# Optimization experiments

Measured on AMD Instinct MI355X. Metric: run time of the kernel, lower is better.

The kernel has to match this reference:

```python
import jax, jax.numpy as jnp
import numpy as np

B, S, D = 4, 2048, 1024
H, DK, DV = 16, 64, 64


def setup_inputs() -> dict:
    key = jax.random.key(0)
    ks = jax.random.split(key, 12)
    s = 0.02
    return {
        "inputEmbeddings_Q": jax.random.normal(ks[0], (B, S, D), jnp.float32),
        "inputEmbeddings_K": jax.random.normal(ks[1], (B, S, D), jnp.float32),
        "inputEmbeddings_V": jax.random.normal(ks[2], (B, S, D), jnp.float32),
        "attentionMask": jax.random.randint(ks[3], (B, S, S), 0, 2) > 0,
        "Wq": jax.random.normal(ks[4], (D, H * DK), jnp.float32) * s,
        "bq": jnp.zeros((H * DK,), jnp.float32),
        "Wk": jax.random.normal(ks[5], (D, H * DK), jnp.float32) * s,
        "bk": jnp.zeros((H * DK,), jnp.float32),
        "Wv": jax.random.normal(ks[6], (D, H * DV), jnp.float32) * s,
        "bv": jnp.zeros((H * DV,), jnp.float32),
        "Wo": jax.random.normal(ks[7], (H * DV, D), jnp.float32) * s,
        "bo": jnp.zeros((D,), jnp.float32),
        "ln_gamma": jnp.ones((D,), jnp.float32),
        "ln_beta": jnp.zeros((D,), jnp.float32),
    }


def _layer_norm(x, gamma, beta, eps=1e-5):
    mu = jnp.mean(x, axis=-1, keepdims=True)
    var = jnp.var(x, axis=-1, keepdims=True)
    return (x - mu) * jax.lax.rsqrt(var + eps) * gamma + beta


def reference(inputEmbeddings_Q, inputEmbeddings_K, inputEmbeddings_V, attentionMask,
              Wq, bq, Wk, bk, Wv, bv, Wo, bo, ln_gamma, ln_beta):
    residual = inputEmbeddings_Q
    b = inputEmbeddings_Q.shape[0]
    # projections -> [B, H, S, d]
    q = (inputEmbeddings_Q @ Wq + bq).reshape(b, -1, H, DK).transpose(0, 2, 1, 3)
    k = (inputEmbeddings_K @ Wk + bk).reshape(b, -1, H, DK).transpose(0, 2, 1, 3)
    v = (inputEmbeddings_V @ Wv + bv).reshape(b, -1, H, DV).transpose(0, 2, 1, 3)
    scores = jnp.einsum("bhqd,bhkd->bhqk", q, k) / np.sqrt(DK).astype(np.float32)
    scores = jnp.where(attentionMask[:, None, :, :], jnp.float32(-1e9), scores)
    attention = jax.nn.softmax(scores, axis=-1)  # [B,H,Sq,Sk]
    context = jnp.einsum("bhqk,bhkd->bhqd", attention, v)
    context = context.transpose(0, 2, 1, 3).reshape(b, -1, H * DV)
    output = context @ Wo + bo
    output = _layer_norm(output + residual, ln_gamma, ln_beta)
    return output, attention
```

## Files before the change

### kernel.cpp

```cpp
#include <hip/hip_runtime.h>

typedef unsigned short u16;
typedef unsigned int u32;
typedef __bf16 bf16x8 __attribute__((ext_vector_type(8)));
typedef __bf16 bf16x4 __attribute__((ext_vector_type(4)));
typedef u16 u16x8 __attribute__((ext_vector_type(8)));
typedef u32 u32x2 __attribute__((ext_vector_type(2)));
typedef u32 u32x4 __attribute__((ext_vector_type(4)));
typedef float f32x4 __attribute__((ext_vector_type(4)));

#define Ss 2048
#define Hh 16

#define WAITV(n) asm volatile("s_waitcnt vmcnt(" #n ")" ::: "memory")
#define BAR() __builtin_amdgcn_s_barrier()
#define SCHED0() __builtin_amdgcn_sched_barrier(0)

__device__ __forceinline__ void gll16(const void* g, void* l) {
  __builtin_amdgcn_global_load_lds((const __attribute__((address_space(1))) void*)g,
                                   (__attribute__((address_space(3))) void*)l, 16, 0, 0);
}

__device__ __forceinline__ bf16x8 lds8(const u16* base, int byteoff) {
  return __builtin_bit_cast(bf16x8, *(const u16x8*)((const char*)base + byteoff));
}
__device__ __forceinline__ bf16x4 lds4(const u16* base, int byteoff) {
  return __builtin_bit_cast(bf16x4, *(const unsigned long long*)((const char*)base + byteoff));
}
__device__ __forceinline__ bf16x8 g8(const u16* p) {
  return __builtin_bit_cast(bf16x8, *(const u16x8*)p);
}
__device__ __forceinline__ u16 bfbits(float f) {
  return __builtin_bit_cast(u16, (__bf16)f);
}

__global__ __launch_bounds__(256) void convert_x(const float* __restrict__ xq,
                                                 const float* __restrict__ xk,
                                                 const float* __restrict__ xv,
                                                 u16* __restrict__ dst) {
  int z = blockIdx.y;
  const float* src = (z == 0) ? xq : ((z == 1) ? xk : xv);
  u16* d = dst + (size_t)z * (8192ull * 1024);
  size_t i = ((size_t)blockIdx.x * 256 + threadIdx.x) * 8;
  float4 v0 = *(const float4*)(src + i);
  float4 v1 = *(const float4*)(src + i + 4);
  bf16x8 o;
  o[0] = (__bf16)v0.x; o[1] = (__bf16)v0.y; o[2] = (__bf16)v0.z; o[3] = (__bf16)v0.w;
  o[4] = (__bf16)v1.x; o[5] = (__bf16)v1.y; o[6] = (__bf16)v1.z; o[7] = (__bf16)v1.w;
  *(bf16x8*)(d + i) = o;
}

__global__ __launch_bounds__(256) void conv_w(const float* __restrict__ wq,
                                              const float* __restrict__ wk,
                                              const float* __restrict__ wv,
                                              const float* __restrict__ wo,
                                              u16* __restrict__ wt) {
  int z = blockIdx.z;
  const float* W = (z == 0) ? wq : (z == 1) ? wk : (z == 2) ? wv : wo;
  u16* O = wt + (size_t)z * (1024ull * 1024);
  __shared__ float tile[64][65];
  int tk = blockIdx.x * 64, tn = blockIdx.y * 64;
  int t = threadIdx.x;
#pragma unroll
  for (int p = 0; p < 4; ++p) {
    int idx = p * 256 + t;
    int r = idx >> 4, c4 = (idx & 15) << 2;
    float4 v = *(const float4*)(W + (size_t)(tk + r) * 1024 + tn + c4);
    tile[r][c4 + 0] = v.x; tile[r][c4 + 1] = v.y;
    tile[r][c4 + 2] = v.z; tile[r][c4 + 3] = v.w;
  }
  __syncthreads();
#pragma unroll
  for (int p = 0; p < 4; ++p) {
    int idx = p * 256 + t;
    int n = idx >> 4, k4 = (idx & 15) << 2;
    bf16x4 o;
    o[0] = (__bf16)tile[k4 + 0][n]; o[1] = (__bf16)tile[k4 + 1][n];
    o[2] = (__bf16)tile[k4 + 2][n]; o[3] = (__bf16)tile[k4 + 3][n];
    *(bf16x4*)(O + (size_t)(tn + n) * 1024 + tk + k4) = o;
  }
}

__global__ __launch_bounds__(256) void pack_mask(const int* __restrict__ m,
                                                 u32* __restrict__ bits) {
  size_t base = (size_t)blockIdx.x * 512;
  int t = threadIdx.x;
  int w = t >> 6, lane = t & 63;
  bool v0 = (m[base + t] != 0);
  bool v1 = (m[base + 256 + t] != 0);
  unsigned long long b0 = __ballot(v0);
  unsigned long long b1 = __ballot(v1);
  size_t wbase = (base >> 5) + (w << 1);
  if (lane == 0) {
    bits[wbase] = (u32)b0;
    bits[wbase + 8] = (u32)b1;
  } else if (lane == 32) {
    bits[wbase + 1] = (u32)(b0 >> 32);
    bits[wbase + 9] = (u32)(b1 >> 32);
  }
}

__global__ __launch_bounds__(256) void gemm_qkv(const u16* __restrict__ Xbf,
                                                const u16* __restrict__ Wt,
                                                const float* __restrict__ bq,
                                                const float* __restrict__ bk,
                                                const float* __restrict__ bv,
                                                u16* __restrict__ OutQK,
                                                u16* __restrict__ Vt) {
  int z = blockIdx.z;
  const u16* A = Xbf + (size_t)z * (8192ull * 1024);
  const u16* Bw = Wt + (size_t)z * (1024ull * 1024);
  const float* bias = (z == 0) ? bq : ((z == 1) ? bk : bv);
  u16* O = OutQK + (size_t)z * (8192ull * 1024);
  float scale = (z == 0) ? (0.125f * 1.4426950408889634f) : 1.0f;

  __shared__ __attribute__((aligned(16))) u16 SM[16384];

  int t = threadIdx.x, w = t >> 6, l = t & 63, lg = l >> 4, lr = l & 15;
  int n_ = blockIdx.x;
  int cx = n_ & 7, slot = n_ >> 3;
  int m0 = (((slot >> 3) << 3) | cx) * 128;
  int n0 = (slot & 7) * 128;
  int wm = (w >> 1) * 64, wn = (w & 1) * 64;

  f32x4 acc[4][4] = {};

#define STAGE_AB(kt_, buf_)                                                    \
  {                                                                            \
    _Pragma("unroll") for (int i = 0; i < 2; ++i) {                            \
      int c = t + i * 256;                                                     \
      int d = c << 4;                                                          \
      int row = d >> 6, off = d & 63;                                          \
      int soff = off ^ ((row & 3) << 4);                                       \
      gll16(A + (size_t)(m0 + row) * 1024 + (kt_) + (soff >> 1),               \
            (char*)SM + (buf_)*8192 + d);                                      \
      gll16(Bw + (size_t)(n0 + row) * 1024 + (kt_) + (soff >> 1),              \
            (char*)SM + 16384 + (buf_)*8192 + d);                              \
    }                                                                          \
  }

  STAGE_AB(0, 0);

  for (int tt = 0; tt < 32; ++tt) {
    int cur = tt & 1;
    if (tt < 31) {
      STAGE_AB((tt + 1) * 32, cur ^ 1);
      WAITV(4);
    } else {
      WAITV(0);
    }
    SCHED0();
    BAR();
    const u16* Ac = SM + cur * 4096;
    const u16* Bc = SM + 8192 + cur * 4096;
    bf16x8 af[4], bfr[4];
#pragma unroll
    for (int mf = 0; mf < 4; ++mf) {
      int row = wm + mf * 16 + lr;
      af[mf] = lds8(Ac, (row << 6) + ((lg ^ (row & 3)) << 4));
    }
#pragma unroll
    for (int nf = 0; nf < 4; ++nf) {
      int row = wn + nf * 16 + lr;
      bfr[nf] = lds8(Bc, (row << 6) + ((lg ^ (row & 3)) << 4));
    }
#pragma unroll
    for (int mf = 0; mf < 4; ++mf)
#pragma unroll
      for (int nf = 0; nf < 4; ++nf)
        acc[mf][nf] = __builtin_amdgcn_mfma_f32_16x16x32_bf16(af[mf], bfr[nf], acc[mf][nf], 0, 0, 0);
    BAR();
  }
#undef STAGE_AB

  if (z == 2) {
#pragma unroll
    for (int mf = 0; mf < 4; ++mf)
#pragma unroll
      for (int nf = 0; nf < 4; ++nf) {
        int mloc = wm + mf * 16 + lg * 4;
        int nloc = wn + nf * 16 + lr;
        bf16x4 ov;
        int n = n0 + nloc;
#pragma unroll
        for (int r = 0; r < 4; ++r) ov[r] = (__bf16)(acc[mf][nf][r] + bias[n]);
        *(bf16x4*)&SM[nloc * 128 + (mloc ^ ((nloc & 7) << 3))] = ov;
      }
    BAR();
    int b_ = m0 >> 11, s0_ = m0 & 2047;
#pragma unroll
    for (int i = 0; i < 8; ++i) {
      int idx = i * 256 + t;
      int nloc = idx >> 4, c = idx & 15;
      u16x8 val = *(const u16x8*)&SM[nloc * 128 + (((c ^ (nloc & 7)) << 3))];
      int n = n0 + nloc, hh = n >> 6, dd = n & 63;
      *(u16x8*)&Vt[(((size_t)(b_ * 16 + hh)) * 64 + dd) * 2048 + s0_ + c * 8] = val;
    }
  } else {
#pragma unroll
    for (int mf = 0; mf < 4; ++mf)
#pragma unroll
      for (int nf = 0; nf < 4; ++nf)
#pragma unroll
        for (int r = 0; r < 4; ++r) {
          int row = wm + mf * 16 + lg * 4 + r;
          int col = wn + nf * 16 + lr;
          float v = (acc[mf][nf][r] + bias[n0 + col]) * scale;
          SM[row * 128 + (col ^ ((row & 7) << 3))] = bfbits(v);
        }
    BAR();
    int b_ = m0 >> 11, s0_ = m0 & 2047;
#pragma unroll
    for (int i = 0; i < 8; ++i) {
      int idx = i * 256 + t;
      int row = idx >> 4, c = idx & 15;
      u16x8 val = *(const u16x8*)&SM[row * 128 + (((c ^ (row & 7)) << 3))];
      int n = n0 + c * 8, hh = n >> 6, dd = n & 63;
      *(u16x8*)&O[(((size_t)(b_ * 16 + hh)) * 2048 + s0_ + row) * 64 + dd] = val;
    }
  }
}

__global__ __launch_bounds__(256, 4) void attn_kernel(const u16* __restrict__ Qs,
                                                      const u16* __restrict__ Ks,
                                                      const u16* __restrict__ Vt,
                                                      const u32* __restrict__ Mbits,
                                                      float* __restrict__ attn,
                                                      u16* __restrict__ Ctx) {
  int bid = blockIdx.x;
  int xcd = bid & 7, j = bid >> 3;
  int bh = xcd * 8 + (j >> 5);
  int q0 = (j & 31) * 64;
  int b = bh >> 4, h = bh & 15;
  int t = threadIdx.x;
  int w = t >> 6, l = t & 63, lg = l >> 4, lr = l & 15;

  const u16* Qb = Qs + (size_t)bh * (Ss * 64);
  const u16* Kb = Ks + (size_t)bh * (Ss * 64);
  const u16* Vb = Vt + (size_t)bh * (64 * Ss);
  int qrow = w * 16 + lr;
  const u32* Mrow = Mbits + ((size_t)b * Ss + q0 + qrow) * 64;

  __shared__ __attribute__((aligned(16))) char SMb[40960];
  u16* Pl = (u16*)(SMb + 32768);

  int srow = t >> 3;
  int skoff = (((t & 7) << 4) ^ ((srow & 7) << 4));

#define STAGE_K2(kc_, buf_)                                                    \
  {                                                                            \
    _Pragma("unroll") for (int i = 0; i < 4; ++i)                              \
        gll16(Kb + (size_t)((kc_) + srow + 32 * i) * 64 + (skoff >> 1),        \
              SMb + (buf_)*16384 + i * 4096 + (t << 4));                       \
  }
#define STAGE_K(kc_, buf_)                                                     \
  {                                                                            \
    gll16(Kb + (size_t)((kc_) + srow) * 64 + (skoff >> 1),                     \
          SMb + (buf_)*8192 + (t << 4));                                       \
    gll16(Kb + (size_t)((kc_) + srow + 32) * 64 + (skoff >> 1),                \
          SMb + (buf_)*8192 + (t << 4) + 4096);                                \
  }
#define STAGE_V(kc_, buf_)                                                     \
  {                                                                            \
    gll16(Vb + (size_t)srow * 2048 + (kc_) + (skoff >> 1),                     \
          SMb + 16384 + (buf_)*8192 + (t << 4));                               \
    gll16(Vb + (size_t)(srow + 32) * 2048 + (kc_) + (skoff >> 1),              \
          SMb + 16384 + (buf_)*8192 + (t << 4) + 4096);                        \
  }

  bf16x8 qf[2];
  {
    const u16* qr = Qb + (size_t)(q0 + qrow) * 64;
    qf[0] = g8(qr + lg * 8);
    qf[1] = g8(qr + 32 + lg * 8);
  }

  int swzq = (lr & 7) << 4;

  float rsum = 0.f;
  {
    STAGE_K2(0, 0);
    u32x4 mq = *(const u32x4*)(Mrow);
    u32x4 mqn;
    for (int tt = 0; tt < 16; ++tt) {
      int cur = tt & 1;
      if (tt < 15) {
        STAGE_K2((tt + 1) * 128, cur ^ 1);
        mqn = *(const u32x4*)(Mrow + ((tt + 1) << 2));
        WAITV(5);
      } else {
        WAITV(0);
      }
      SCHED0();
      BAR();
      const u16* Kc = (const u16*)(SMb + cur * 16384);
#pragma unroll
      for (int nf = 0; nf < 8; ++nf) {
        int krow = nf * 16 + lr;
        int base = krow << 7, swz = (krow & 7) << 4;
        f32x4 sc = {};
        __builtin_amdgcn_s_setprio(1);
        sc = __builtin_amdgcn_mfma_f32_16x16x32_bf16(
            lds8(Kc, base + ((lg << 4) ^ swz)), qf[0], sc, 0, 0, 0);
        sc = __builtin_amdgcn_mfma_f32_16x16x32_bf16(
            lds8(Kc, base + ((64 + (lg << 4)) ^ swz)), qf[1], sc, 0, 0, 0);
        __builtin_amdgcn_s_setprio(0);
        u32 mb = mq[nf >> 1] >> (((nf & 1) << 4) + (lg << 2));
#pragma unroll
        for (int r = 0; r < 4; ++r)
          rsum += ((mb >> r) & 1) ? 0.f : __builtin_amdgcn_exp2f(sc[r]);
      }
      mq = mqn;
      BAR();
    }
  }
  float inv;
  {
    float s = rsum;
    s += __shfl_xor(s, 16);
    s += __shfl_xor(s, 32);
    inv = 1.0f / s;
  }

  float* abase = attn + ((size_t)bh * Ss + q0 + w * 16) * Ss;
  int rsub = l >> 4;
  int kch = (l & 15);
  f32x4 ctx[4] = {};
  {
    STAGE_K(0, 0);
    STAGE_V(0, 0);
    u32x2 mq = *(const u32x2*)(Mrow);
    u32x2 mqn;
    for (int tt = 0; tt < 32; ++tt) {
      int cur = tt & 1;
      if (tt == 0) {
        STAGE_K(64, 1);
        STAGE_V(64, 1);
        mqn = *(const u32x2*)(Mrow + 2);
        WAITV(5);
      } else if (tt < 31) {
        STAGE_K((tt + 1) * 64, cur ^ 1);
        STAGE_V((tt + 1) * 64, cur ^ 1);
        mqn = *(const u32x2*)(Mrow + ((tt + 1) << 1));
        WAITV(9);
      } else {
        WAITV(4);
      }
      SCHED0();
      BAR();
      const u16* Kc = (const u16*)(SMb + cur * 8192);
      const u16* Vc = (const u16*)(SMb + 16384 + cur * 8192);
      int kc = tt * 64;
#pragma unroll
      for (int nf = 0; nf < 4; ++nf) {
        int krow = nf * 16 + lr;
        int base = krow << 7, swz = (krow & 7) << 4;
        f32x4 sc = {};
        __builtin_amdgcn_s_setprio(1);
        sc = __builtin_amdgcn_mfma_f32_16x16x32_bf16(
            lds8(Kc, base + ((lg << 4) ^ swz)), qf[0], sc, 0, 0, 0);
        sc = __builtin_amdgcn_mfma_f32_16x16x32_bf16(
            lds8(Kc, base + ((64 + (lg << 4)) ^ swz)), qf[1], sc, 0, 0, 0);
        __builtin_amdgcn_s_setprio(0);
        u32 mb = mq[nf >> 1] >> (((nf & 1) << 4) + (lg << 2));
        f32x4 p4;
#pragma unroll
        for (int r = 0; r < 4; ++r)
          p4[r] = (((mb >> r) & 1) ? 0.f : __builtin_amdgcn_exp2f(sc[r])) * inv;
        bf16x4 pb;
#pragma unroll
        for (int r = 0; r < 4; ++r) pb[r] = (__bf16)p4[r];
        *(bf16x4*)((char*)Pl + (qrow << 7) + (((nf << 5) + (lg << 3)) ^ swzq)) = pb;
      }
#pragma unroll
      for (int rb = 0; rb < 4; ++rb) {
        int rrow = rb * 4 + rsub;
        int R = w * 16 + rrow;
        bf16x4 pv4 = lds4(Pl, (R << 7) + ((kch << 3) ^ ((R & 7) << 4)));
        f32x4 o4;
#pragma unroll
        for (int r = 0; r < 4; ++r) o4[r] = (float)pv4[r];
        __builtin_nontemporal_store(
            o4, (f32x4*)(abase + (size_t)rrow * Ss + kc + kch * 4));
      }
      __builtin_amdgcn_s_setprio(1);
#pragma unroll
      for (int ks = 0; ks < 2; ++ks) {
        bf16x8 pf = lds8(Pl, (qrow << 7) + (((ks << 6) + (lg << 4)) ^ swzq));
#pragma unroll
        for (int nfo = 0; nfo < 4; ++nfo) {
          int vr = nfo * 16 + lr;
          bf16x8 vf = lds8(Vc,
                           (vr << 7) + (((ks << 6) + (lg << 4)) ^ ((vr & 7) << 4)));
          ctx[nfo] = __builtin_amdgcn_mfma_f32_16x16x32_bf16(pf, vf, ctx[nfo], 0, 0, 0);
        }
      }
      __builtin_amdgcn_s_setprio(0);
      mq = mqn;
      BAR();
    }
  }
#undef STAGE_K2
#undef STAGE_K
#undef STAGE_V

  {
    u16* Cl = (u16*)SMb + w * 1024;
#pragma unroll
    for (int nfo = 0; nfo < 4; ++nfo)
#pragma unroll
      for (int r = 0; r < 4; ++r)
        Cl[(lg * 4 + r) * 64 + nfo * 16 + lr] = bfbits(ctx[nfo][r]);
#pragma unroll
    for (int i = 0; i < 2; ++i) {
      int row = (l >> 3) + (i << 3);
      u16x8 cv = *(const u16x8*)(Cl + row * 64 + (l & 7) * 8);
      *(u16x8*)&Ctx[((size_t)b * Ss + q0 + w * 16 + row) * 1024 + h * 64 +
                    (l & 7) * 8] = cv;
    }
  }
}

__global__ __launch_bounds__(256) void gemm_out(const u16* __restrict__ Ctx,
                                                const u16* __restrict__ Wot,
                                                const float* __restrict__ bo,
                                                const float* __restrict__ resid,
                                                float* __restrict__ preLN) {
  __shared__ __attribute__((aligned(16))) u16 Al[2][128 * 32];
  __shared__ __attribute__((aligned(16))) u16 Bl[2][128 * 32];

  int t = threadIdx.x, w = t >> 6, l = t & 63, lg = l >> 4, lr = l & 15;
  int n_ = blockIdx.x;
  int cx = n_ & 7, slot = n_ >> 3;
  int m0 = (((slot >> 3) << 3) | cx) * 128;
  int n0 = (slot & 7) * 128;
  int wm = (w >> 1) * 64, wn = (w & 1) * 64;

  f32x4 acc[4][4] = {};

#define STAGE_AB(kt_, buf_)                                                    \
  {                                                                            \
    _Pragma("unroll") for (int i = 0; i < 2; ++i) {                            \
      int c = t + i * 256;                                                     \
      int d = c << 4;                                                          \
      int row = d >> 6, off = d & 63;                                          \
      int soff = off ^ ((row & 3) << 4);                                       \
      gll16(Ctx + (size_t)(m0 + row) * 1024 + (kt_) + (soff >> 1),             \
            (char*)Al[buf_] + d);                                              \
      gll16(Wot + (size_t)(n0 + row) * 1024 + (kt_) + (soff >> 1),             \
            (char*)Bl[buf_] + d);                                              \
    }                                                                          \
  }

  STAGE_AB(0, 0);

  for (int tt = 0; tt < 32; ++tt) {
    int cur = tt & 1;
    if (tt < 31) {
      STAGE_AB((tt + 1) * 32, cur ^ 1);
      WAITV(4);
    } else {
      WAITV(0);
    }
    SCHED0();
    BAR();
    bf16x8 af[4], bfr[4];
#pragma unroll
    for (int mf = 0; mf < 4; ++mf) {
      int row = wm + mf * 16 + lr;
      af[mf] = lds8(Al[cur], (row << 6) + ((lg ^ (row & 3)) << 4));
    }
#pragma unroll
    for (int nf = 0; nf < 4; ++nf) {
      int row = wn + nf * 16 + lr;
      bfr[nf] = lds8(Bl[cur], (row << 6) + ((lg ^ (row & 3)) << 4));
    }
#pragma unroll
    for (int mf = 0; mf < 4; ++mf)
#pragma unroll
      for (int nf = 0; nf < 4; ++nf)
        acc[mf][nf] = __builtin_amdgcn_mfma_f32_16x16x32_bf16(af[mf], bfr[nf], acc[mf][nf], 0, 0, 0);
    BAR();
  }
#undef STAGE_AB

#pragma unroll
  for (int mf = 0; mf < 4; ++mf)
#pragma unroll
    for (int nf = 0; nf < 4; ++nf)
#pragma unroll
      for (int r = 0; r < 4; ++r) {
        int m = m0 + wm + mf * 16 + lg * 4 + r;
        int n = n0 + wn + nf * 16 + lr;
        float v = acc[mf][nf][r] + bo[n] + resid[(size_t)m * 1024 + n];
        preLN[(size_t)m * 1024 + n] = v;
      }
}

__global__ __launch_bounds__(256) void layernorm(const float* __restrict__ x,
                                                 const float* __restrict__ gamma,
                                                 const float* __restrict__ beta,
                                                 float* __restrict__ out) {
  int t = threadIdx.x;
  int w = t >> 6, l = t & 63;
  int row = blockIdx.x * 4 + w;
  const float* xr = x + (size_t)row * 1024;
  float4 v[4];
  float s = 0.f, s2 = 0.f;
#pragma unroll
  for (int c = 0; c < 4; ++c) {
    v[c] = *(const float4*)(xr + c * 256 + l * 4);
    s += v[c].x + v[c].y + v[c].z + v[c].w;
    s2 += v[c].x * v[c].x + v[c].y * v[c].y + v[c].z * v[c].z + v[c].w * v[c].w;
  }
#pragma unroll
  for (int m = 1; m < 64; m <<= 1) {
    s += __shfl_xor(s, m);
    s2 += __shfl_xor(s2, m);
  }
  float mu = s * (1.0f / 1024.0f);
  float var = s2 * (1.0f / 1024.0f) - mu * mu;
  float rs = rsqrtf(var + 1e-5f);
  float* orow = out + (size_t)row * 1024;
#pragma unroll
  for (int c = 0; c < 4; ++c) {
    float4 g = *(const float4*)(gamma + c * 256 + l * 4);
    float4 bb = *(const float4*)(beta + c * 256 + l * 4);
    float4 o;
    o.x = (v[c].x - mu) * rs * g.x + bb.x;
    o.y = (v[c].y - mu) * rs * g.y + bb.y;
    o.z = (v[c].z - mu) * rs * g.z + bb.z;
    o.w = (v[c].w - mu) * rs * g.w + bb.w;
    *(float4*)(orow + c * 256 + l * 4) = o;
  }
}

extern "C" void kernel_launch(void* const* d_in, const int* in_sizes, int n_in,
                              void* d_out, int out_size, void* d_ws, size_t ws_size,
                              hipStream_t stream) {
  const float* Xq = (const float*)d_in[0];
  const float* Xk = (const float*)d_in[1];
  const float* Xv = (const float*)d_in[2];
  const int* Mask = (const int*)d_in[3];
  const float* Wq = (const float*)d_in[4];
  const float* bq = (const float*)d_in[5];
  const float* Wk = (const float*)d_in[6];
  const float* bk = (const float*)d_in[7];
  const float* Wv = (const float*)d_in[8];
  const float* bv = (const float*)d_in[9];
  const float* Wo = (const float*)d_in[10];
  const float* bo = (const float*)d_in[11];
  const float* gamma = (const float*)d_in[12];
  const float* beta = (const float*)d_in[13];

  char* ws = (char*)d_ws;
  u16* Xbf   = (u16*)(ws + 0);
  u16* Wt    = (u16*)(ws + 50331648);
  u16* Qs    = (u16*)(ws + 58720256);
  u16* Vt    = (u16*)(ws + 92274688);
  u32* Mbits = (u32*)(ws + 109051904);
  u16* Ctx   = (u16*)(ws + 111149056);
  float* preLN = (float*)(ws + 0);

  u16* Ks = Qs + 8192ull * 1024;

  float* outp = (float*)d_out;
  float* attn = outp + 8388608ull;

  (void)in_sizes; (void)n_in; (void)out_size; (void)ws_size;

  convert_x<<<dim3(4096, 3), 256, 0, stream>>>(Xq, Xk, Xv, Xbf);
  conv_w<<<dim3(16, 16, 4), 256, 0, stream>>>(Wq, Wk, Wv, Wo, Wt);
  pack_mask<<<32768, 256, 0, stream>>>(Mask, Mbits);
  gemm_qkv<<<dim3(512, 1, 3), 256, 0, stream>>>(Xbf, Wt, bq, bk, bv, Qs, Vt);
  attn_kernel<<<2048, 256, 0, stream>>>(Qs, Ks, Vt, Mbits, attn, Ctx);
  gemm_out<<<512, 256, 0, stream>>>(Ctx, Wt + 3ull * 1048576, bo, Xq, preLN);
  layernorm<<<2048, 256, 0, stream>>>(preLN, gamma, beta, outp);
}
```

Baseline: 390.5 us.

## Merge prep kernels into one launch and store pre-LayerNorm output as bf16

Combines the input conversion, weight transpose-conversion and mask packing into a single kernel dispatched by block index, with nontemporal loads for the K/V inputs and the mask. gemm_out now stages its tile through LDS, adds the residual with coalesced vector loads, and writes the pre-LayerNorm values as bf16 instead of fp32. LayerNorm reads the bf16 buffer. This removes two launches and halves the pre-LN traffic, but rounding to bf16 twice before the normalisation lowers accuracy.

```diff
diff --git a/kernel.cpp b/kernel.cpp
--- a/kernel.cpp
+++ b/kernel.cpp
@@ -34,69 +34,77 @@
   return __builtin_bit_cast(u16, (__bf16)f);
 }
 
-__global__ __launch_bounds__(256) void convert_x(const float* __restrict__ xq,
-                                                 const float* __restrict__ xk,
-                                                 const float* __restrict__ xv,
-                                                 u16* __restrict__ dst) {
-  int z = blockIdx.y;
-  const float* src = (z == 0) ? xq : ((z == 1) ? xk : xv);
-  u16* d = dst + (size_t)z * (8192ull * 1024);
-  size_t i = ((size_t)blockIdx.x * 256 + threadIdx.x) * 8;
-  float4 v0 = *(const float4*)(src + i);
-  float4 v1 = *(const float4*)(src + i + 4);
-  bf16x8 o;
-  o[0] = (__bf16)v0.x; o[1] = (__bf16)v0.y; o[2] = (__bf16)v0.z; o[3] = (__bf16)v0.w;
-  o[4] = (__bf16)v1.x; o[5] = (__bf16)v1.y; o[6] = (__bf16)v1.z; o[7] = (__bf16)v1.w;
-  *(bf16x8*)(d + i) = o;
-}
-
-__global__ __launch_bounds__(256) void conv_w(const float* __restrict__ wq,
-                                              const float* __restrict__ wk,
-                                              const float* __restrict__ wv,
-                                              const float* __restrict__ wo,
-                                              u16* __restrict__ wt) {
-  int z = blockIdx.z;
-  const float* W = (z == 0) ? wq : (z == 1) ? wk : (z == 2) ? wv : wo;
-  u16* O = wt + (size_t)z * (1024ull * 1024);
+__global__ __launch_bounds__(256) void prep(const float* __restrict__ xq,
+                                            const float* __restrict__ xk,
+                                            const float* __restrict__ xv,
+                                            const float* __restrict__ wq,
+                                            const float* __restrict__ wk,
+                                            const float* __restrict__ wv,
+                                            const float* __restrict__ wo,
+                                            const int* __restrict__ mask,
+                                            u16* __restrict__ Xbf,
+                                            u16* __restrict__ wt,
+                                            u32* __restrict__ bits) {
   __shared__ float tile[64][65];
-  int tk = blockIdx.x * 64, tn = blockIdx.y * 64;
+  int bid = blockIdx.x;
   int t = threadIdx.x;
-#pragma unroll
-  for (int p = 0; p < 4; ++p) {
-    int idx = p * 256 + t;
-    int r = idx >> 4, c4 = (idx & 15) << 2;
-    float4 v = *(const float4*)(W + (size_t)(tk + r) * 1024 + tn + c4);
-    tile[r][c4 + 0] = v.x; tile[r][c4 + 1] = v.y;
-    tile[r][c4 + 2] = v.z; tile[r][c4 + 3] = v.w;
-  }
-  __syncthreads();
-#pragma unroll
-  for (int p = 0; p < 4; ++p) {
-    int idx = p * 256 + t;
-    int n = idx >> 4, k4 = (idx & 15) << 2;
-    bf16x4 o;
-    o[0] = (__bf16)tile[k4 + 0][n]; o[1] = (__bf16)tile[k4 + 1][n];
-    o[2] = (__bf16)tile[k4 + 2][n]; o[3] = (__bf16)tile[k4 + 3][n];
-    *(bf16x4*)(O + (size_t)(tn + n) * 1024 + tk + k4) = o;
-  }
-}
-
-__global__ __launch_bounds__(256) void pack_mask(const int* __restrict__ m,
-                                                 u32* __restrict__ bits) {
-  size_t base = (size_t)blockIdx.x * 512;
-  int t = threadIdx.x;
-  int w = t >> 6, lane = t & 63;
-  bool v0 = (m[base + t] != 0);
-  bool v1 = (m[base + 256 + t] != 0);
-  unsigned long long b0 = __ballot(v0);
-  unsigned long long b1 = __ballot(v1);
-  size_t wbase = (base >> 5) + (w << 1);
-  if (lane == 0) {
-    bits[wbase] = (u32)b0;
-    bits[wbase + 8] = (u32)b1;
-  } else if (lane == 32) {
-    bits[wbase + 1] = (u32)(b0 >> 32);
-    bits[wbase + 9] = (u32)(b1 >> 32);
+  if (bid < 12288) {
+    int z = bid >> 12;
+    int sub = bid & 4095;
+    const float* src = (z == 0) ? xq : ((z == 1) ? xk : xv);
+    u16* d = Xbf + (size_t)z * (8192ull * 1024);
+    size_t i = ((size_t)sub * 256 + t) * 8;
+    f32x4 v0, v1;
+    if (z == 0) {
+      v0 = *(const f32x4*)(src + i);
+      v1 = *(const f32x4*)(src + i + 4);
+    } else {
+      v0 = __builtin_nontemporal_load((const f32x4*)(src + i));
+      v1 = __builtin_nontemporal_load((const f32x4*)(src + i + 4));
+    }
+    bf16x8 o;
+    o[0] = (__bf16)v0[0]; o[1] = (__bf16)v0[1]; o[2] = (__bf16)v0[2]; o[3] = (__bf16)v0[3];
+    o[4] = (__bf16)v1[0]; o[5] = (__bf16)v1[1]; o[6] = (__bf16)v1[2]; o[7] = (__bf16)v1[3];
+    *(bf16x8*)(d + i) = o;
+  } else if (bid < 13312) {
+    int idx = bid - 12288;
+    int z = idx >> 8;
+    const float* W = (z == 0) ? wq : (z == 1) ? wk : (z == 2) ? wv : wo;
+    u16* O = wt + (size_t)z * (1024ull * 1024);
+    int tk = (idx & 15) * 64, tn = ((idx >> 4) & 15) * 64;
+#pragma unroll
+    for (int p = 0; p < 4; ++p) {
+      int id2 = p * 256 + t;
+      int r = id2 >> 4, c4 = (id2 & 15) << 2;
+      f32x4 v = *(const f32x4*)(W + (size_t)(tk + r) * 1024 + tn + c4);
+      tile[r][c4 + 0] = v[0]; tile[r][c4 + 1] = v[1];
+      tile[r][c4 + 2] = v[2]; tile[r][c4 + 3] = v[3];
+    }
+    __syncthreads();
+#pragma unroll
+    for (int p = 0; p < 4; ++p) {
+      int id2 = p * 256 + t;
+      int n = id2 >> 4, k4 = (id2 & 15) << 2;
+      bf16x4 o;
+      o[0] = (__bf16)tile[k4 + 0][n]; o[1] = (__bf16)tile[k4 + 1][n];
+      o[2] = (__bf16)tile[k4 + 2][n]; o[3] = (__bf16)tile[k4 + 3][n];
+      *(bf16x4*)(O + (size_t)(tn + n) * 1024 + tk + k4) = o;
+    }
+  } else {
+    size_t base = (size_t)(bid - 13312) * 512;
+    int w = t >> 6, lane = t & 63;
+    bool v0 = (__builtin_nontemporal_load(&mask[base + t]) != 0);
+    bool v1 = (__builtin_nontemporal_load(&mask[base + 256 + t]) != 0);
+    unsigned long long b0 = __ballot(v0);
+    unsigned long long b1 = __ballot(v1);
+    size_t wbase = (base >> 5) + (w << 1);
+    if (lane == 0) {
+      bits[wbase] = (u32)b0;
+      bits[wbase + 8] = (u32)b1;
+    } else if (lane == 32) {
+      bits[wbase + 1] = (u32)(b0 >> 32);
+      bits[wbase + 9] = (u32)(b1 >> 32);
+    }
   }
 }
 
@@ -425,9 +433,8 @@
                                                 const u16* __restrict__ Wot,
                                                 const float* __restrict__ bo,
                                                 const float* __restrict__ resid,
-                                                float* __restrict__ preLN) {
-  __shared__ __attribute__((aligned(16))) u16 Al[2][128 * 32];
-  __shared__ __attribute__((aligned(16))) u16 Bl[2][128 * 32];
+                                                u16* __restrict__ preLN16) {
+  __shared__ __attribute__((aligned(16))) u16 SM[16384];
 
   int t = threadIdx.x, w = t >> 6, l = t & 63, lg = l >> 4, lr = l & 15;
   int n_ = blockIdx.x;
@@ -446,9 +453,9 @@
       int row = d >> 6, off = d & 63;                                          \
       int soff = off ^ ((row & 3) << 4);                                       \
       gll16(Ctx + (size_t)(m0 + row) * 1024 + (kt_) + (soff >> 1),             \
-            (char*)Al[buf_] + d);                                              \
+            (char*)SM + (buf_)*8192 + d);                                      \
       gll16(Wot + (size_t)(n0 + row) * 1024 + (kt_) + (soff >> 1),             \
-            (char*)Bl[buf_] + d);                                              \
+            (char*)SM + 16384 + (buf_)*8192 + d);                              \
     }                                                                          \
   }
 
@@ -464,16 +471,18 @@
     }
     SCHED0();
     BAR();
+    const u16* Ac = SM + cur * 4096;
+    const u16* Bc = SM + 8192 + cur * 4096;
     bf16x8 af[4], bfr[4];
 #pragma unroll
     for (int mf = 0; mf < 4; ++mf) {
       int row = wm + mf * 16 + lr;
-      af[mf] = lds8(Al[cur], (row << 6) + ((lg ^ (row & 3)) << 4));
+      af[mf] = lds8(Ac, (row << 6) + ((lg ^ (row & 3)) << 4));
     }
 #pragma unroll
     for (int nf = 0; nf < 4; ++nf) {
       int row = wn + nf * 16 + lr;
-      bfr[nf] = lds8(Bl[cur], (row << 6) + ((lg ^ (row & 3)) << 4));
+      bfr[nf] = lds8(Bc, (row << 6) + ((lg ^ (row & 3)) << 4));
     }
 #pragma unroll
     for (int mf = 0; mf < 4; ++mf)
@@ -490,28 +499,54 @@
     for (int nf = 0; nf < 4; ++nf)
 #pragma unroll
       for (int r = 0; r < 4; ++r) {
-        int m = m0 + wm + mf * 16 + lg * 4 + r;
-        int n = n0 + wn + nf * 16 + lr;
-        float v = acc[mf][nf][r] + bo[n] + resid[(size_t)m * 1024 + n];
-        preLN[(size_t)m * 1024 + n] = v;
-      }
-}
-
-__global__ __launch_bounds__(256) void layernorm(const float* __restrict__ x,
+        int row = wm + mf * 16 + lg * 4 + r;
+        int col = wn + nf * 16 + lr;
+        float v = acc[mf][nf][r] + bo[n0 + col];
+        SM[row * 128 + (col ^ ((row & 7) << 3))] = bfbits(v);
+      }
+  BAR();
+#pragma unroll
+  for (int i = 0; i < 8; ++i) {
+    int idx = i * 256 + t;
+    int row = idx >> 4, c = idx & 15;
+    u16x8 val = *(const u16x8*)&SM[row * 128 + (((c ^ (row & 7)) << 3))];
+    bf16x8 vb = __builtin_bit_cast(bf16x8, val);
+    const float* rr = resid + (size_t)(m0 + row) * 1024 + n0 + c * 8;
+    f32x4 f0 = *(const f32x4*)rr;
+    f32x4 f1 = *(const f32x4*)(rr + 4);
+    bf16x8 o;
+    o[0] = (__bf16)((float)vb[0] + f0[0]);
+    o[1] = (__bf16)((float)vb[1] + f0[1]);
+    o[2] = (__bf16)((float)vb[2] + f0[2]);
+    o[3] = (__bf16)((float)vb[3] + f0[3]);
+    o[4] = (__bf16)((float)vb[4] + f1[0]);
+    o[5] = (__bf16)((float)vb[5] + f1[1]);
+    o[6] = (__bf16)((float)vb[6] + f1[2]);
+    o[7] = (__bf16)((float)vb[7] + f1[3]);
+    *(bf16x8*)&preLN16[(size_t)(m0 + row) * 1024 + n0 + c * 8] = o;
+  }
+}
+
+__global__ __launch_bounds__(256) void layernorm(const u16* __restrict__ x16,
                                                  const float* __restrict__ gamma,
                                                  const float* __restrict__ beta,
                                                  float* __restrict__ out) {
   int t = threadIdx.x;
   int w = t >> 6, l = t & 63;
   int row = blockIdx.x * 4 + w;
-  const float* xr = x + (size_t)row * 1024;
-  float4 v[4];
+  const u16* xr = x16 + (size_t)row * 1024;
+  float xv[16];
   float s = 0.f, s2 = 0.f;
 #pragma unroll
-  for (int c = 0; c < 4; ++c) {
-    v[c] = *(const float4*)(xr + c * 256 + l * 4);
-    s += v[c].x + v[c].y + v[c].z + v[c].w;
-    s2 += v[c].x * v[c].x + v[c].y * v[c].y + v[c].z * v[c].z + v[c].w * v[c].w;
+  for (int c = 0; c < 2; ++c) {
+    bf16x8 v = g8(xr + c * 512 + l * 8);
+#pragma unroll
+    for (int j = 0; j < 8; ++j) {
+      float f = (float)v[j];
+      xv[c * 8 + j] = f;
+      s += f;
+      s2 += f * f;
+    }
   }
 #pragma unroll
   for (int m = 1; m < 64; m <<= 1) {
@@ -523,15 +558,18 @@
   float rs = rsqrtf(var + 1e-5f);
   float* orow = out + (size_t)row * 1024;
 #pragma unroll
-  for (int c = 0; c < 4; ++c) {
-    float4 g = *(const float4*)(gamma + c * 256 + l * 4);
-    float4 bb = *(const float4*)(beta + c * 256 + l * 4);
-    float4 o;
-    o.x = (v[c].x - mu) * rs * g.x + bb.x;
-    o.y = (v[c].y - mu) * rs * g.y + bb.y;
-    o.z = (v[c].z - mu) * rs * g.z + bb.z;
-    o.w = (v[c].w - mu) * rs * g.w + bb.w;
-    *(float4*)(orow + c * 256 + l * 4) = o;
+  for (int c = 0; c < 2; ++c) {
+#pragma unroll
+    for (int q = 0; q < 2; ++q) {
+      int off = c * 512 + l * 8 + q * 4;
+      f32x4 g = *(const f32x4*)(gamma + off);
+      f32x4 bb = *(const f32x4*)(beta + off);
+      f32x4 o;
+#pragma unroll
+      for (int j = 0; j < 4; ++j)
+        o[j] = (xv[c * 8 + q * 4 + j] - mu) * rs * g[j] + bb[j];
+      *(f32x4*)(orow + off) = o;
+    }
   }
 }
 
@@ -560,7 +598,7 @@
   u16* Vt    = (u16*)(ws + 92274688);
   u32* Mbits = (u32*)(ws + 109051904);
   u16* Ctx   = (u16*)(ws + 111149056);
-  float* preLN = (float*)(ws + 0);
+  u16* preLN16 = (u16*)(ws + 0);
 
   u16* Ks = Qs + 8192ull * 1024;
 
@@ -569,11 +607,9 @@
 
   (void)in_sizes; (void)n_in; (void)out_size; (void)ws_size;
 
-  convert_x<<<dim3(4096, 3), 256, 0, stream>>>(Xq, Xk, Xv, Xbf);
-  conv_w<<<dim3(16, 16, 4), 256, 0, stream>>>(Wq, Wk, Wv, Wo, Wt);
-  pack_mask<<<32768, 256, 0, stream>>>(Mask, Mbits);
+  prep<<<46080, 256, 0, stream>>>(Xq, Xk, Xv, Wq, Wk, Wv, Wo, Mask, Xbf, Wt, Mbits);
   gemm_qkv<<<dim3(512, 1, 3), 256, 0, stream>>>(Xbf, Wt, bq, bk, bv, Qs, Vt);
   attn_kernel<<<2048, 256, 0, stream>>>(Qs, Ks, Vt, Mbits, attn, Ctx);
-  gemm_out<<<512, 256, 0, stream>>>(Ctx, Wt + 3ull * 1048576, bo, Xq, preLN);
-  layernorm<<<2048, 256, 0, stream>>>(preLN, gamma, beta, outp);
-}
+  gemm_out<<<512, 256, 0, stream>>>(Ctx, Wt + 3ull * 1048576, bo, Xq, preLN16);
+  layernorm<<<2048, 256, 0, stream>>>(preLN16, gamma, beta, outp);
+}
```

Result: faster. 380.0 us (-2.7%).
